# Kernel optimization log

Measured on AMD Instinct MI355X. Metric: run time of the kernel, lower is better.

## Reference

```python
import jax, jax.numpy as jnp
import numpy as np
from jax import lax

EPS = 1e-5      # BatchNorm1d default eps
SLOPE = 0.01    # LeakyReLU default negative_slope
DN = ('NCDHW', 'OIDHW', 'NCDHW')
PAD_31 = ((1, 1), (0, 0), (1, 1))   # kernel (3,1,3), padding (1,0,1)
PAD_13 = ((0, 0), (1, 1), (1, 1))   # kernel (1,3,3), padding (0,1,1)
PAD_P = ((1, 1), (1, 1), (1, 1))    # pool kernel 3, padding 1
STRIDE_P = (2, 2, 1)                # height_pooling=False -> stride (2,2,1)


def setup_inputs() -> dict:
    key = jax.random.key(0)
    ks = jax.random.split(key, 8)
    B, Cin, Cout = 1, 32, 64
    D1, D2, D3 = 160, 160, 32
    mask = jax.random.randint(ks[0], (B, 1, D1, D2, D3), 0, 2) > 0
    x = jax.random.normal(ks[1], (B, Cin, D1, D2, D3), dtype=jnp.float32)

    def w(k, cin, cout, kd, kh, kw):
        return jax.random.normal(k, (cout, cin, kd, kh, kw), dtype=jnp.float32) * 0.05

    inp = {
        'x': x, 'mask': mask,
        'W_A1': w(ks[2], Cin, Cout, 3, 1, 3),
        'W_A2': w(ks[3], Cout, Cout, 1, 3, 3),
        'W_B1': w(ks[4], Cin, Cout, 1, 3, 3),
        'W_B2': w(ks[5], Cout, Cout, 3, 1, 3),
        'W_pool': w(ks[6], Cout, Cout, 3, 3, 3),
    }
    for name in ('A1', 'A2', 'B1', 'B2'):
        inp['g_' + name] = jnp.ones((Cout,), jnp.float32)
        inp['b_' + name] = jnp.zeros((Cout,), jnp.float32)
    return inp


def _conv(h, W, pad, stride=(1, 1, 1)):
    return lax.conv_general_dilated(h, W, stride, pad, dimension_numbers=DN)


def _lrelu(h):
    return jnp.where(h >= 0, h, SLOPE * h)


def _masked_bn(h, m, n_active, gamma, beta):
    # BatchNorm1d over the [N_active, C] sparse feature tensor:
    # per-channel stats over active voxels only (biased variance, training mode).
    mean = jnp.sum(h * m, axis=(0, 2, 3, 4)) / n_active
    mu = mean[None, :, None, None, None]
    var = jnp.sum(((h - mu) ** 2) * m, axis=(0, 2, 3, 4)) / n_active
    inv = lax.rsqrt(var + EPS)[None, :, None, None, None]
    out = (h - mu) * inv * gamma[None, :, None, None, None] + beta[None, :, None, None, None]
    return out * m  # keep inactive sites exactly zero


def reference(x, mask, W_A1, W_A2, W_B1, W_B2, W_pool,
              g_A1, b_A1, g_A2, b_A2, g_B1, b_B1, g_B2, b_B2):
    m = mask.astype(x.dtype)                      # [B,1,D1,D2,D3] active-site indicator
    n_active = jnp.sum(m)
    xs = x * m                                    # sparse input: zero at inactive voxels

    def subm(h, W, pad):
        # submanifold conv: compute only at active output sites (same site set as input)
        return _conv(h, W, pad) * m

    # branch A: conv3x1 -> LeakyReLU -> BN -> conv1x3 -> LeakyReLU -> BN
    res_A = _masked_bn(_lrelu(subm(xs, W_A1, PAD_31)), m, n_active, g_A1, b_A1)
    res_A = _masked_bn(_lrelu(subm(res_A, W_A2, PAD_13)), m, n_active, g_A2, b_A2)

    # branch B: conv1x3 -> LeakyReLU -> BN -> conv3x1 -> LeakyReLU -> BN
    res_B = _masked_bn(_lrelu(subm(xs, W_B1, PAD_13)), m, n_active, g_B1, b_B1)
    res_B = _masked_bn(_lrelu(subm(res_B, W_B2, PAD_31)), m, n_active, g_B2, b_B2)

    res_B = res_B + res_A

    # strided SparseConv3d pool: output active where any input in 3x3x3 window is active
    ones_k = jnp.ones((1, 1, 3, 3, 3), x.dtype)
    out_mask = (_conv(m, ones_k, PAD_P, STRIDE_P) > 0).astype(x.dtype)
    down = _conv(res_B, W_pool, PAD_P, STRIDE_P) * out_mask
    return (down, res_B)
```

## Files before the change

kernel.cpp:

```cpp
#include <hip/hip_runtime.h>

static constexpr int ND1=160, ND2=160, ND3=32;
static constexpr int SP  = ND1*ND2*ND3;
static constexpr int CO  = 64;
static constexpr int OD1=80, OD2=80, OD3=32;
static constexpr int OSP = OD1*OD2*OD3;
static constexpr int NSC = 64;

typedef __attribute__((ext_vector_type(8))) short  short8;
typedef __attribute__((ext_vector_type(4))) float  f32x4;

__device__ __forceinline__ float b2f(unsigned u){ return __uint_as_float(u<<16); }
__device__ __forceinline__ unsigned short f2b(float f){
    unsigned u = __float_as_uint(f);
    u += 0x7fffu + ((u>>16)&1u);
    return (unsigned short)(u>>16);
}

__global__ void k_detect(const unsigned char* __restrict__ mb, int* __restrict__ flag)
{
    __shared__ int lf;
    if (threadIdx.x == 0) lf = 0;
    __syncthreads();
    int f = 0;
    for (int i = blockIdx.x*256 + threadIdx.x; i < SP; i += gridDim.x*256) {
        unsigned char b = mb[i];
        if (b > 1) f |= 4;
        if (b != 0 && (i & 3)) f |= 1;
    }
    if (f) atomicOr(&lf, f);
    __syncthreads();
    if (threadIdx.x == 0 && lf) atomicOr(flag, lf);
}

__global__ void k_mask(const void* __restrict__ mraw, const int* __restrict__ flag,
                       float* __restrict__ m, float* __restrict__ nactN)
{
    int i = blockIdx.x*256 + threadIdx.x;
    int f = *flag;
    float v;
    if (f & 4)      v = (reinterpret_cast<const float*>(mraw)[i] != 0.f) ? 1.f : 0.f;
    else if (f & 1) v = (reinterpret_cast<const unsigned char*>(mraw)[i] != 0) ? 1.f : 0.f;
    else            v = (reinterpret_cast<const int*>(mraw)[i] != 0) ? 1.f : 0.f;
    m[i] = v;
    float s = v;
    #pragma unroll
    for (int off = 32; off > 0; off >>= 1) s += __shfl_xor(s, off);
    __shared__ float wsum[4];
    if ((threadIdx.x & 63) == 0) wsum[threadIdx.x >> 6] = s;
    __syncthreads();
    if (threadIdx.x == 0) atomicAdd(&nactN[blockIdx.x & (NSC-1)], wsum[0]+wsum[1]+wsum[2]+wsum[3]);
}

__global__ void k_outmask(const float* __restrict__ m, float* __restrict__ om)
{
    int i = blockIdx.x*256 + threadIdx.x;
    int o3 = i & 31; int t = i >> 5; int o2 = t % OD2; int o1 = t / OD2;
    float s = 0.f;
    for (int kd = 0; kd < 3; kd++) { int d1 = 2*o1 - 1 + kd; if ((unsigned)d1 >= ND1) continue;
      for (int kh = 0; kh < 3; kh++) { int d2 = 2*o2 - 1 + kh; if ((unsigned)d2 >= ND2) continue;
        for (int kw = 0; kw < 3; kw++) { int d3 = o3 - 1 + kw; if ((unsigned)d3 >= ND3) continue;
          s += m[(d1*ND2 + d2)*ND3 + d3];
        } } }
    om[i] = (s > 0.f) ? 1.f : 0.f;
}

__global__ void k_finalize2(const float* __restrict__ SN0, const float* __restrict__ g0,
                            const float* __restrict__ b0, float* __restrict__ o0,
                            const float* __restrict__ SN1, const float* __restrict__ g1,
                            const float* __restrict__ b1, float* __restrict__ o1,
                            const float* __restrict__ nactN)
{
    const float* SN = blockIdx.x ? SN1 : SN0;
    const float* g  = blockIdx.x ? g1  : g0;
    const float* b  = blockIdx.x ? b1  : b0;
    float*       o  = blockIdx.x ? o1  : o0;
    int c = threadIdx.x;
    float s1 = 0.f, s2 = 0.f;
    #pragma unroll 4
    for (int k = 0; k < NSC; k++){
        s1 += SN[k*128 + c];
        s2 += SN[k*128 + 64 + c];
    }
    float nn = nactN[c];
    #pragma unroll
    for (int off = 32; off > 0; off >>= 1) nn += __shfl_xor(nn, off);
    float mean = s1 / nn;
    float var  = s2 / nn - mean*mean;
    float inv  = rsqrtf(var + 1e-5f);
    float sc   = inv * g[c];
    o[c]      = sc;
    o[64 + c] = b[c] - mean*sc;
}

__global__ void k_wprep(const float* __restrict__ W, unsigned short* __restrict__ Wt,
                        int CIN, int NT)
{
    int i = blockIdx.x*256 + threadIdx.x;
    int K = CIN*NT;
    if (i >= 64*K) return;
    int ksub = i & 31;
    int t = i >> 5;
    int co = t & 63;
    int kc = t >> 6;
    int nch = CIN >> 5;
    int tap = kc / nch;
    int ci  = (kc - tap*nch)*32 + ksub;
    Wt[i] = f2b(W[((size_t)co*CIN + ci)*NT + tap]);
}

__global__ void k_prep_x(const float* __restrict__ x, const float* __restrict__ m,
                         unsigned short* __restrict__ xt)
{
    __shared__ float t[64][33];
    int sp0 = blockIdx.x*64;
    int tid = threadIdx.x;
    int c = tid>>6, s = tid&63;
    float mm = m[sp0+s];
    #pragma unroll
    for (int r=0;r<8;r++){
        int ci = c + r*4;
        t[s][ci] = x[(size_t)ci*SP + sp0 + s]*mm;
    }
    __syncthreads();
    int sp = tid>>2, c0 = (tid&3)*8;
    unsigned short o[8];
    #pragma unroll
    for (int i=0;i<8;i++) o[i] = f2b(t[sp][c0+i]);
    uint4 pk;
    pk.x = o[0] | ((unsigned)o[1]<<16);
    pk.y = o[2] | ((unsigned)o[3]<<16);
    pk.z = o[4] | ((unsigned)o[5]<<16);
    pk.w = o[6] | ((unsigned)o[7]<<16);
    *reinterpret_cast<uint4*>(xt + (size_t)(sp0+sp)*32 + c0) = pk;
}

__global__ void k_resB(const unsigned short* __restrict__ hA, const unsigned short* __restrict__ hB,
                       const float* __restrict__ sA, const float* __restrict__ sB,
                       const float* __restrict__ m,
                       unsigned short* __restrict__ rbt, float* __restrict__ resf)
{
    __shared__ float t[64][65];
    __shared__ float ss[256];
    int tid = threadIdx.x;
    if (tid < 128){ ss[tid] = sA[tid]; ss[128+tid] = sB[tid]; }
    __syncthreads();
    int sp0 = blockIdx.x*64;
    int sp = tid>>2, c0 = (tid&3)*16;
    float mm = m[sp0+sp];
    const size_t base = (size_t)(sp0+sp)*64 + c0;
    uint4 a0 = *reinterpret_cast<const uint4*>(hA + base);
    uint4 a1 = *reinterpret_cast<const uint4*>(hA + base + 8);
    uint4 b0 = *reinterpret_cast<const uint4*>(hB + base);
    uint4 b1 = *reinterpret_cast<const uint4*>(hB + base + 8);
    unsigned ua[16] = {a0.x&0xffffu,a0.x>>16,a0.y&0xffffu,a0.y>>16,a0.z&0xffffu,a0.z>>16,a0.w&0xffffu,a0.w>>16,
                       a1.x&0xffffu,a1.x>>16,a1.y&0xffffu,a1.y>>16,a1.z&0xffffu,a1.z>>16,a1.w&0xffffu,a1.w>>16};
    unsigned ub[16] = {b0.x&0xffffu,b0.x>>16,b0.y&0xffffu,b0.y>>16,b0.z&0xffffu,b0.z>>16,b0.w&0xffffu,b0.w>>16,
                       b1.x&0xffffu,b1.x>>16,b1.y&0xffffu,b1.y>>16,b1.z&0xffffu,b1.z>>16,b1.w&0xffffu,b1.w>>16};
    unsigned short o[16];
    #pragma unroll
    for (int q=0;q<16;q++){
        int ci = c0+q;
        float v = (b2f(ua[q])*ss[ci] + ss[64+ci] + b2f(ub[q])*ss[128+ci] + ss[192+ci])*mm;
        t[sp][ci] = v;
        o[q] = f2b(v);
    }
    uint4 p0, p1;
    p0.x = o[0]|((unsigned)o[1]<<16);  p0.y = o[2]|((unsigned)o[3]<<16);
    p0.z = o[4]|((unsigned)o[5]<<16);  p0.w = o[6]|((unsigned)o[7]<<16);
    p1.x = o[8]|((unsigned)o[9]<<16);  p1.y = o[10]|((unsigned)o[11]<<16);
    p1.z = o[12]|((unsigned)o[13]<<16); p1.w = o[14]|((unsigned)o[15]<<16);
    *reinterpret_cast<uint4*>(rbt + base)     = p0;
    *reinterpret_cast<uint4*>(rbt + base + 8) = p1;
    __syncthreads();
    int ci = tid>>2, s0 = (tid&3)*16;
    #pragma unroll
    for (int kq=0;kq<4;kq++){
        float4 ov;
        ov.x = t[s0+4*kq+0][ci]; ov.y = t[s0+4*kq+1][ci];
        ov.z = t[s0+4*kq+2][ci]; ov.w = t[s0+4*kq+3][ci];
        *reinterpret_cast<float4*>(resf + (size_t)ci*SP + sp0 + s0 + 4*kq) = ov;
    }
}

template<int KIND, int CIN, bool HASAFF>
__launch_bounds__(256, (CIN==32) ? 3 : 2)
__global__ void mconv10(const unsigned short* __restrict__ in,
                        const unsigned short* __restrict__ Wt,
                        const float* __restrict__ scsh,
                        const float* __restrict__ mstage,
                        const float* __restrict__ mout,
                        unsigned short* __restrict__ outb,
                        float* __restrict__ statsN)
{
    constexpr int NCH  = CIN/32;
    constexpr int NKC  = NCH*9;
    constexpr int NR   = 10;
    constexpr int ROWB = 34*CIN*2;
    constexpr int SWZ  = (CIN==64) ? 7 : 3;
    __shared__ __align__(16) char lds[NR*ROWB];
    __shared__ float sst[128];

    const int tid = threadIdx.x;
    const int w = tid>>6, l = tid&63, g = l>>4, lj = l&15;
    const int h = w&1, rg = w>>1;

    int gi = (blockIdx.x & 7)*(gridDim.x>>3) + (blockIdx.x>>3);
    int z  = gi % 160;
    int r0 = (gi / 160)*8;

    if (tid < 128) sst[tid] = 0.f;

    const int sd3 = tid>>3;
    const int k0  = (tid&7)*(CIN/8);

    float sc[8], sh[8];
    if (HASAFF){
        #pragma unroll
        for (int j=0;j<8;j++){ sc[j]=scsh[k0+j]; sh[j]=scsh[64+k0+j]; }
    }

    for (int i = tid; i < NR*2*(CIN/8); i += 256){
        int per = CIN/8;
        int rr = i / (2*per);
        int rem = i - rr*2*per;
        int slot = (rem >= per) ? 33 : 0;
        int kc16 = (rem >= per) ? (rem - per) : rem;
        int dst = rr*ROWB + slot*CIN*2 + kc16*16;
        dst ^= ((slot&SWZ)<<4);
        *reinterpret_cast<uint4*>(lds + dst) = make_uint4(0,0,0,0);
    }

    if (CIN==64){
        uint4 v[NR]; float mmr[NR];
        #pragma unroll
        for (int rr=0; rr<NR; rr++){
            int rw = r0 - 1 + rr;
            v[rr] = make_uint4(0,0,0,0); mmr[rr] = 0.f;
            if ((unsigned)rw < 160u){
                int vox = (KIND==0) ? ((rw*ND2 + z)*ND3 + sd3)
                                    : ((z*ND2 + rw)*ND3 + sd3);
                v[rr] = *reinterpret_cast<const uint4*>(in + (size_t)vox*CIN + k0);
                if (HASAFF) mmr[rr] = mstage[vox];
            }
        }
        #pragma unroll
        for (int rr=0; rr<NR; rr++){
            uint4 vv = v[rr];
            if (HASAFF){
                float mm = mmr[rr];
                unsigned us[8] = {vv.x&0xffffu,vv.x>>16,vv.y&0xffffu,vv.y>>16,
                                  vv.z&0xffffu,vv.z>>16,vv.w&0xffffu,vv.w>>16};
                unsigned short o[8];
                #pragma unroll
                for (int j=0;j<8;j++) o[j] = f2b((b2f(us[j])*sc[j]+sh[j])*mm);
                vv.x = o[0]|((unsigned)o[1]<<16); vv.y = o[2]|((unsigned)o[3]<<16);
                vv.z = o[4]|((unsigned)o[5]<<16); vv.w = o[6]|((unsigned)o[7]<<16);
            }
            int dst = (rr*ROWB + (((sd3+1)*CIN + k0)*2)) ^ (((sd3+1)&SWZ)<<4);
            *reinterpret_cast<uint4*>(lds + dst) = vv;
        }
    } else {
        uint2 v[NR];
        #pragma unroll
        for (int rr=0; rr<NR; rr++){
            int rw = r0 - 1 + rr;
            v[rr] = make_uint2(0,0);
            if ((unsigned)rw < 160u){
                int vox = (KIND==0) ? ((rw*ND2 + z)*ND3 + sd3)
                                    : ((z*ND2 + rw)*ND3 + sd3);
                v[rr] = *reinterpret_cast<const uint2*>(in + (size_t)vox*CIN + k0);
            }
        }
        #pragma unroll
        for (int rr=0; rr<NR; rr++){
            int dst = (rr*ROWB + (((sd3+1)*CIN + k0)*2)) ^ (((sd3+1)&SWZ)<<4);
            *reinterpret_cast<uint2*>(lds + dst) = v[rr];
        }
    }

    short8 pa[NKC][2];
    {
        const unsigned short* wb = Wt + (size_t)(h*32)*32 + lj*32 + g*8;
        #pragma unroll
        for (int kc=0; kc<NKC; kc++){
            pa[kc][0] = *reinterpret_cast<const short8*>(wb + (size_t)kc*2048);
            pa[kc][1] = *reinterpret_cast<const short8*>(wb + (size_t)kc*2048 + 512);
        }
    }

    int tb[8], ovox[8];
    float mm[8];
    #pragma unroll
    for (int t=0;t<8;t++){
        int rowb = rg*4 + (t>>1);
        int o3   = (t&1)*16 + lj;
        tb[t] = rowb*ROWB + ((o3*CIN + g*8)*2);
        int o2r = r0 + rowb;
        ovox[t] = (KIND==0) ? ((o2r*ND2 + z)*ND3 + o3)
                            : ((z*ND2 + o2r)*ND3 + o3);
        mm[t] = mout[ovox[t]];
    }
    int swz[3];
    #pragma unroll
    for (int kw=0;kw<3;kw++) swz[kw] = ((lj+kw)&SWZ)<<4;

    __syncthreads();

    f32x4 acc[2][8];
    #pragma unroll
    for (int c=0;c<2;c++)
        #pragma unroll
        for (int t=0;t<8;t++)
            #pragma unroll
            for (int q=0;q<4;q++) acc[c][t][q] = 0.f;

    #pragma unroll
    for (int ch=0; ch<NCH; ch++){
        #pragma unroll
        for (int tap=0; tap<9; tap++){
            const int kd = tap/3, kw = tap - kd*3;
            const int kc = tap*NCH + ch;
            const int tapoff = kd*ROWB + (kw*CIN + ch*32)*2;
            #pragma unroll
            for (int t=0;t<8;t++){
                int off = (tb[t] + tapoff) ^ swz[kw];
                short8 bv = *reinterpret_cast<const short8*>(lds + off);
                acc[0][t] = __builtin_amdgcn_mfma_f32_16x16x32_bf16(pa[kc][0], bv, acc[0][t], 0,0,0);
                acc[1][t] = __builtin_amdgcn_mfma_f32_16x16x32_bf16(pa[kc][1], bv, acc[1][t], 0,0,0);
            }
        }
    }

    #pragma unroll
    for (int c=0;c<2;c++){
        const int ct = h*2 + c;
        float s1[4] = {0.f,0.f,0.f,0.f};
        float s2[4] = {0.f,0.f,0.f,0.f};
        #pragma unroll
        for (int t=0;t<8;t++){
            float v[4];
            #pragma unroll
            for (int r=0;r<4;r++){
                float xv = acc[c][t][r]*mm[t];
                xv = (xv >= 0.f) ? xv : 0.01f*xv;
                v[r] = xv; s1[r] += xv; s2[r] += xv*xv;
            }
            unsigned lo = f2b(v[0]) | ((unsigned)f2b(v[1])<<16);
            unsigned hi = f2b(v[2]) | ((unsigned)f2b(v[3])<<16);
            *reinterpret_cast<uint2*>(outb + (size_t)ovox[t]*64 + ct*16 + g*4) = make_uint2(lo,hi);
        }
        #pragma unroll
        for (int r=0;r<4;r++){
            float a = s1[r], b = s2[r];
            a += __shfl_xor(a,1); b += __shfl_xor(b,1);
            a += __shfl_xor(a,2); b += __shfl_xor(b,2);
            a += __shfl_xor(a,4); b += __shfl_xor(b,4);
            a += __shfl_xor(a,8); b += __shfl_xor(b,8);
            if (lj == 0){
                atomicAdd(&sst[ct*16 + g*4 + r], a);
                atomicAdd(&sst[64 + ct*16 + g*4 + r], b);
            }
        }
    }
    __syncthreads();
    if (tid < 128){
        float* sg = statsN + (size_t)(blockIdx.x & (NSC-1))*128;
        atomicAdd(&sg[tid], sst[tid]);
    }
}

__launch_bounds__(256, 2)
__global__ void mpool3(const unsigned short* __restrict__ in,
                       const unsigned short* __restrict__ Wt,
                       const float* __restrict__ mout,
                       float* __restrict__ outf)
{
    constexpr int ROWB = 34*64*2;
    __shared__ __align__(16) char lds[9*ROWB];

    const int tid = threadIdx.x;
    const int w = tid>>6, l = tid&63, g = l>>4, lj = l&15;
    const int h = w&1, rg = w>>1;

    int gi = (blockIdx.x & 7)*(gridDim.x>>3) + (blockIdx.x>>3);
    int z  = gi % OD1;
    int r0 = (gi / OD1)*4;

    const int sd3 = tid>>3;
    const int k0  = (tid&7)*8;

    int swz[3];
    #pragma unroll
    for (int kw=0;kw<3;kw++) swz[kw] = ((lj+kw)&7)<<4;

    for (int i = tid; i < 9*2*8; i += 256){
        int rr = i / 16;
        int rem = i - rr*16;
        int slot = (rem >= 8) ? 33 : 0;
        int kc16 = rem & 7;
        int dst = rr*ROWB + slot*128 + kc16*16;
        dst ^= ((slot&7)<<4);
        *reinterpret_cast<uint4*>(lds + dst) = make_uint4(0,0,0,0);
    }

    int tbl[4], ovx[4];
    float om[4];
    #pragma unroll
    for (int t=0;t<4;t++){
        int row = rg*2 + (t>>1);
        int o3  = (t&1)*16 + lj;
        tbl[t] = (o3*64 + g*8)*2;
        ovx[t] = (z*OD2 + (r0 + row))*OD3 + o3;
        om[t]  = mout[ovx[t]];
    }

    f32x4 acc[2][4];
    #pragma unroll
    for (int c=0;c<2;c++)
        #pragma unroll
        for (int t=0;t<4;t++)
            #pragma unroll
            for (int q=0;q<4;q++) acc[c][t][q] = 0.f;

    const unsigned short* wb = Wt + (size_t)(h*32)*32 + lj*32 + g*8;

    uint4 rv[9];
    short8 pa[18][2];

    #pragma unroll 1
    for (int kd=0; kd<3; kd++){
        {
            int d1 = 2*z - 1 + kd;
            bool pok = ((unsigned)d1 < (unsigned)ND1);
            #pragma unroll
            for (int rr=0; rr<9; rr++){
                int d2 = 2*r0 - 1 + rr;
                rv[rr] = make_uint4(0,0,0,0);
                if (pok && ((unsigned)d2 < (unsigned)ND2)){
                    int vox = (d1*ND2 + d2)*ND3 + sd3;
                    rv[rr] = *reinterpret_cast<const uint4*>(in + (size_t)vox*64 + k0);
                }
            }
        }
        #pragma unroll
        for (int i=0;i<18;i++){
            const int ch = i/9, tap = i - (i/9)*9;
            const int kc = (kd*9 + tap)*2 + ch;
            pa[i][0] = *reinterpret_cast<const short8*>(wb + (size_t)kc*2048);
            pa[i][1] = *reinterpret_cast<const short8*>(wb + (size_t)kc*2048 + 512);
        }
        __syncthreads();
        #pragma unroll
        for (int rr=0; rr<9; rr++){
            int dst = (rr*ROWB + (((sd3+1)*64 + k0)*2)) ^ (((sd3+1)&7)<<4);
            *reinterpret_cast<uint4*>(lds + dst) = rv[rr];
        }
        __syncthreads();
        #pragma unroll
        for (int ch=0; ch<2; ch++){
            #pragma unroll
            for (int tap=0; tap<9; tap++){
                const int kh = tap/3, kw = tap - (tap/3)*3;
                const int pi = ch*9 + tap;
                #pragma unroll
                for (int t=0;t<4;t++){
                    const int rowl = 2*(rg*2 + (t>>1)) + kh;
                    int off = (rowl*ROWB + (kw*64 + ch*32)*2 + tbl[t]) ^ swz[kw];
                    short8 bv = *reinterpret_cast<const short8*>(lds + off);
                    acc[0][t] = __builtin_amdgcn_mfma_f32_16x16x32_bf16(pa[pi][0], bv, acc[0][t], 0,0,0);
                    acc[1][t] = __builtin_amdgcn_mfma_f32_16x16x32_bf16(pa[pi][1], bv, acc[1][t], 0,0,0);
                }
            }
        }
    }
    #pragma unroll
    for (int c=0;c<2;c++){
        const int ct = h*2 + c;
        #pragma unroll
        for (int t=0;t<4;t++){
            #pragma unroll
            for (int r=0;r<4;r++){
                int co = ct*16 + g*4 + r;
                outf[(size_t)co*OSP + ovx[t]] = acc[c][t][r]*om[t];
            }
        }
    }
}

extern "C" void kernel_launch(void* const* d_in, const int* in_sizes, int n_in,
                              void* d_out, int out_size, void* d_ws, size_t ws_size,
                              hipStream_t stream)
{
    const float* x      = (const float*)d_in[0];
    const void*  mraw   = d_in[1];
    const float* W_A1   = (const float*)d_in[2];
    const float* W_A2   = (const float*)d_in[3];
    const float* W_B1   = (const float*)d_in[4];
    const float* W_B2   = (const float*)d_in[5];
    const float* W_pool = (const float*)d_in[6];
    const float* g_A1 = (const float*)d_in[7],  *b_A1 = (const float*)d_in[8];
    const float* g_A2 = (const float*)d_in[9],  *b_A2 = (const float*)d_in[10];
    const float* g_B1 = (const float*)d_in[11], *b_B1 = (const float*)d_in[12];
    const float* g_B2 = (const float*)d_in[13], *b_B2 = (const float*)d_in[14];

    char* p = (char*)d_ws;
    float* m     = (float*)p; p += (size_t)SP*4;
    float* omask = (float*)p; p += (size_t)OSP*4;
    float* statsN= (float*)p; p += 4*NSC*128*4;
    float* scsh  = (float*)p; p += 4*128*4;
    float* nactN = (float*)p; p += NSC*4;
    int*   flag  = (int*)p;   p += 4;
    p += 252;
    unsigned short* WtA1 = (unsigned short*)p; p += 288*64*2;
    unsigned short* WtA2 = (unsigned short*)p; p += 576*64*2;
    unsigned short* WtB1 = (unsigned short*)p; p += 288*64*2;
    unsigned short* WtB2 = (unsigned short*)p; p += 576*64*2;
    unsigned short* WtP  = (unsigned short*)p; p += 1728*64*2;
    unsigned short* X = (unsigned short*)p; p += (size_t)SP*32*2;
    unsigned short* P = (unsigned short*)p; p += (size_t)SP*64*2;
    unsigned short* Q = (unsigned short*)p; p += (size_t)SP*64*2;
    unsigned short* R = (unsigned short*)p; p += (size_t)SP*64*2;

    float* down = (float*)d_out;
    float* resf = down + (size_t)CO*OSP;

    hipMemsetAsync(statsN, 0, (4*NSC*128 + 4*128 + NSC)*4 + 4, stream);
    k_detect<<<256, 256, 0, stream>>>((const unsigned char*)mraw, flag);
    k_mask<<<SP/256, 256, 0, stream>>>(mraw, flag, m, nactN);
    k_outmask<<<OSP/256, 256, 0, stream>>>(m, omask);
    k_prep_x<<<SP/64, 256, 0, stream>>>(x, m, X);

    k_wprep<<<(64*288+255)/256, 256, 0, stream>>>(W_A1, WtA1, 32, 9);
    k_wprep<<<(64*576+255)/256, 256, 0, stream>>>(W_A2, WtA2, 64, 9);
    k_wprep<<<(64*288+255)/256, 256, 0, stream>>>(W_B1, WtB1, 32, 9);
    k_wprep<<<(64*576+255)/256, 256, 0, stream>>>(W_B2, WtB2, 64, 9);
    k_wprep<<<(64*1728+255)/256, 256, 0, stream>>>(W_pool, WtP, 64, 27);

    float* SA1 = statsN + 0*NSC*128;
    float* SA2 = statsN + 1*NSC*128;
    float* SB1 = statsN + 2*NSC*128;
    float* SB2 = statsN + 3*NSC*128;

    mconv10<0,32,false><<<3200, 256, 0, stream>>>(X, WtA1, nullptr, nullptr, m, P, SA1);
    mconv10<1,32,false><<<3200, 256, 0, stream>>>(X, WtB1, nullptr, nullptr, m, Q, SB1);
    k_finalize2<<<2, 64, 0, stream>>>(SA1, g_A1, b_A1, scsh + 0,
                                      SB1, g_B1, b_B1, scsh + 256, nactN);
    mconv10<1,64,true><<<3200, 256, 0, stream>>>(P, WtA2, scsh + 0,   m, m, R, SA2);
    mconv10<0,64,true><<<3200, 256, 0, stream>>>(Q, WtB2, scsh + 256, m, m, P, SB2);
    k_finalize2<<<2, 64, 0, stream>>>(SA2, g_A2, b_A2, scsh + 128,
                                      SB2, g_B2, b_B2, scsh + 384, nactN);
    k_resB<<<SP/64, 256, 0, stream>>>(R, P, scsh + 128, scsh + 384, m, Q, resf);
    mpool3<<<1600, 256, 0, stream>>>(Q, WtP, omask, down);
}
```

Before: 699.4 us.

## Restructure pool conv to stage all depth rows per channel half

The strided pool convolution now loops over two 32-channel halves instead of three depth slices. Each pass loads all 27 input rows (3 depth by 9 height) into a larger dynamically sized LDS buffer, using padded 80-byte slots in place of the XOR swizzle. This halves the number of load/barrier phases and issues more global loads per phase. In exchange it uses about 73 KB of LDS per block, which may limit how many blocks fit per CU, and uses narrower 8-byte global loads.

```diff
diff --git a/kernel.cpp b/kernel.cpp
--- a/kernel.cpp
+++ b/kernel.cpp
@@ -371,13 +371,14 @@
 }
 
 __launch_bounds__(256, 2)
-__global__ void mpool3(const unsigned short* __restrict__ in,
+__global__ void mpool4(const unsigned short* __restrict__ in,
                        const unsigned short* __restrict__ Wt,
                        const float* __restrict__ mout,
                        float* __restrict__ outf)
 {
-    constexpr int ROWB = 34*64*2;
-    __shared__ __align__(16) char lds[9*ROWB];
+    constexpr int SLOTB = 80;
+    constexpr int ROWB  = 34*SLOTB;
+    extern __shared__ __align__(16) char lds[];
 
     const int tid = threadIdx.x;
     const int w = tid>>6, l = tid&63, g = l>>4, lj = l&15;
@@ -388,29 +389,21 @@
     int r0 = (gi / OD1)*4;
 
     const int sd3 = tid>>3;
-    const int k0  = (tid&7)*8;
-
-    int swz[3];
-    #pragma unroll
-    for (int kw=0;kw<3;kw++) swz[kw] = ((lj+kw)&7)<<4;
-
-    for (int i = tid; i < 9*2*8; i += 256){
-        int rr = i / 16;
-        int rem = i - rr*16;
-        int slot = (rem >= 8) ? 33 : 0;
-        int kc16 = rem & 7;
-        int dst = rr*ROWB + slot*128 + kc16*16;
-        dst ^= ((slot&7)<<4);
-        *reinterpret_cast<uint4*>(lds + dst) = make_uint4(0,0,0,0);
-    }
-
-    int tbl[4], ovx[4];
+    const int kq  = tid&7;
+
+    for (int i = tid; i < 27*2*4; i += 256){
+        int row = i >> 3, rem = i & 7;
+        int slot = (rem >= 4) ? 33 : 0;
+        int c16 = rem & 3;
+        *reinterpret_cast<uint4*>(lds + row*ROWB + slot*SLOTB + c16*16) = make_uint4(0,0,0,0);
+    }
+
+    int ovx[4];
     float om[4];
     #pragma unroll
     for (int t=0;t<4;t++){
         int row = rg*2 + (t>>1);
         int o3  = (t&1)*16 + lj;
-        tbl[t] = (o3*64 + g*8)*2;
         ovx[t] = (z*OD2 + (r0 + row))*OD3 + o3;
         om[t]  = mout[ovx[t]];
     }
@@ -423,57 +416,54 @@
             #pragma unroll
             for (int q=0;q<4;q++) acc[c][t][q] = 0.f;
 
-    const unsigned short* wb = Wt + (size_t)(h*32)*32 + lj*32 + g*8;
-
-    uint4 rv[9];
-    short8 pa[18][2];
+    const unsigned short* wbase = Wt + (size_t)(h*32)*32 + lj*32 + g*8;
 
     #pragma unroll 1
-    for (int kd=0; kd<3; kd++){
-        {
+    for (int ph=0; ph<2; ph++){
+        uint2 v[27];
+        #pragma unroll
+        for (int i=0;i<27;i++){
+            const int kd = i/9, rr = i - (i/9)*9;
             int d1 = 2*z - 1 + kd;
-            bool pok = ((unsigned)d1 < (unsigned)ND1);
-            #pragma unroll
-            for (int rr=0; rr<9; rr++){
-                int d2 = 2*r0 - 1 + rr;
-                rv[rr] = make_uint4(0,0,0,0);
-                if (pok && ((unsigned)d2 < (unsigned)ND2)){
-                    int vox = (d1*ND2 + d2)*ND3 + sd3;
-                    rv[rr] = *reinterpret_cast<const uint4*>(in + (size_t)vox*64 + k0);
-                }
-            }
-        }
-        #pragma unroll
-        for (int i=0;i<18;i++){
-            const int ch = i/9, tap = i - (i/9)*9;
-            const int kc = (kd*9 + tap)*2 + ch;
-            pa[i][0] = *reinterpret_cast<const short8*>(wb + (size_t)kc*2048);
-            pa[i][1] = *reinterpret_cast<const short8*>(wb + (size_t)kc*2048 + 512);
+            int d2 = 2*r0 - 1 + rr;
+            v[i] = make_uint2(0,0);
+            if ((unsigned)d1 < (unsigned)ND1 && (unsigned)d2 < (unsigned)ND2){
+                int vox = (d1*ND2 + d2)*ND3 + sd3;
+                v[i] = *reinterpret_cast<const uint2*>(in + (size_t)vox*64 + ph*32 + kq*4);
+            }
         }
         __syncthreads();
         #pragma unroll
-        for (int rr=0; rr<9; rr++){
-            int dst = (rr*ROWB + (((sd3+1)*64 + k0)*2)) ^ (((sd3+1)&7)<<4);
-            *reinterpret_cast<uint4*>(lds + dst) = rv[rr];
+        for (int i=0;i<27;i++){
+            *reinterpret_cast<uint2*>(lds + i*ROWB + (sd3+1)*SLOTB + kq*8) = v[i];
         }
         __syncthreads();
-        #pragma unroll
-        for (int ch=0; ch<2; ch++){
+
+        #pragma unroll
+        for (int kd=0; kd<3; kd++){
+            short8 pa[9][2];
+            #pragma unroll
+            for (int tap=0; tap<9; tap++){
+                const int kc = (kd*9 + tap)*2 + ph;
+                pa[tap][0] = *reinterpret_cast<const short8*>(wbase + (size_t)kc*2048);
+                pa[tap][1] = *reinterpret_cast<const short8*>(wbase + (size_t)kc*2048 + 512);
+            }
             #pragma unroll
             for (int tap=0; tap<9; tap++){
                 const int kh = tap/3, kw = tap - (tap/3)*3;
-                const int pi = ch*9 + tap;
                 #pragma unroll
                 for (int t=0;t<4;t++){
-                    const int rowl = 2*(rg*2 + (t>>1)) + kh;
-                    int off = (rowl*ROWB + (kw*64 + ch*32)*2 + tbl[t]) ^ swz[kw];
-                    short8 bv = *reinterpret_cast<const short8*>(lds + off);
-                    acc[0][t] = __builtin_amdgcn_mfma_f32_16x16x32_bf16(pa[pi][0], bv, acc[0][t], 0,0,0);
-                    acc[1][t] = __builtin_amdgcn_mfma_f32_16x16x32_bf16(pa[pi][1], bv, acc[1][t], 0,0,0);
+                    const int rr = 2*(rg*2 + (t>>1)) + kh;
+                    const int slot = (t&1)*16 + lj + kw;
+                    const char* bp = lds + (kd*9 + rr)*ROWB + slot*SLOTB + g*16;
+                    short8 bv = *reinterpret_cast<const short8*>(bp);
+                    acc[0][t] = __builtin_amdgcn_mfma_f32_16x16x32_bf16(pa[tap][0], bv, acc[0][t], 0,0,0);
+                    acc[1][t] = __builtin_amdgcn_mfma_f32_16x16x32_bf16(pa[tap][1], bv, acc[1][t], 0,0,0);
                 }
             }
         }
     }
+
     #pragma unroll
     for (int c=0;c<2;c++){
         const int ct = h*2 + c;
@@ -525,6 +515,9 @@
     float* down = (float*)d_out;
     float* resf = down + (size_t)CO*OSP;
 
+    const int shmP = 27*34*80;
+    hipFuncSetAttribute((const void*)&mpool4, hipFuncAttributeMaxDynamicSharedMemorySize, shmP);
+
     hipMemsetAsync(statsN, 0, (4*NSC*128 + 4*128 + NSC)*4 + 4, stream);
     k_detect<<<256, 256, 0, stream>>>((const unsigned char*)mraw, flag);
     k_mask<<<SP/256, 256, 0, stream>>>(mraw, flag, m, nactN);
@@ -551,5 +544,5 @@
     k_finalize2<<<2, 64, 0, stream>>>(SA2, g_A2, b_A2, scsh + 128,
                                       SB2, g_B2, b_B2, scsh + 384, nactN);
     k_resB<<<SP/64, 256, 0, stream>>>(R, P, scsh + 128, scsh + 384, m, Q, resf);
-    mpool3<<<1600, 256, 0, stream>>>(Q, WtP, omask, down);
-}
+    mpool4<<<1600, 256, shmP, stream>>>(Q, WtP, omask, down);
+}
```

Measured after the change: 667.8 us. -4.5%, faster.
